# Kernel tuning notes

Measured on AMD Instinct MI355X. Metric: run time of the kernel, lower is better.

## Reference

```python
import jax, jax.numpy as jnp
import numpy as np

N = 50000      # nodes
E = 800000     # edges
NIN = 512      # input features
NHID = 128     # hidden
NCLS = 64      # classes


def setup_inputs() -> dict:
    key = jax.random.key(0)
    k0, k1, k2, k3 = jax.random.split(key, 4)
    x = jax.random.normal(k0, (N, NIN), dtype=jnp.float32)
    edge_index = jax.random.randint(k1, (2, E), 0, N, dtype=jnp.int64)
    # Glorot-style init for GCNConv linear weights (bias starts at zero in PyG)
    W1 = jax.random.normal(k2, (NIN, NHID), dtype=jnp.float32) * (1.0 / np.sqrt(NIN))
    W2 = jax.random.normal(k3, (NHID, NCLS), dtype=jnp.float32) * (1.0 / np.sqrt(NHID))
    b1 = jnp.zeros((NHID,), dtype=jnp.float32)
    b2 = jnp.zeros((NCLS,), dtype=jnp.float32)
    return {"x": x, "edge_index": edge_index, "W1": W1, "b1": b1, "W2": W2, "b2": b2}


def gcn_conv(x, W, b, src, dst, n):
    """PyG GCNConv: linear transform, then sym-normalized aggregation with self-loops."""
    xw = x @ W                                                  # [n, out]
    ones = jnp.ones(src.shape[0], dtype=xw.dtype)
    deg = jax.ops.segment_sum(ones, dst, num_segments=n) + 1.0  # +1 for self-loop
    dinv = jax.lax.rsqrt(deg)                                   # deg >= 1
    norm = dinv[src] * dinv[dst]                                # [E]
    agg = jax.ops.segment_sum(xw[src] * norm[:, None], dst, num_segments=n)
    agg = agg + (dinv * dinv)[:, None] * xw                     # self-loop messages
    return agg + b


def reference(x, edge_index, W1, b1, W2, b2):
    src, dst = edge_index[0], edge_index[1]
    n = x.shape[0]
    # eval mode: dropout is a no-op; bn is defined but unused in forward
    h = gcn_conv(x, W1, b1, src, dst, n)
    h = jax.nn.relu(h)
    o = gcn_conv(h, W2, b2, src, dst, n)
    return jax.nn.log_softmax(o, axis=1)
```

## Files before the change

### kernel.cpp

```cpp
#include <hip/hip_runtime.h>
#include <hip/hip_bf16.h>
#include <cstdint>
#include <cstddef>

#define NNODES 50000
#define NEDGES 800000
#define NIN    512
#define NHID   128
#define NCLS   64

#define SCAN_BLK 512
#define SCAN_NB ((NNODES + SCAN_BLK - 1) / SCAN_BLK)

typedef __attribute__((ext_vector_type(8))) short bf16x8;
typedef __attribute__((ext_vector_type(4))) float f32x4;

static __device__ __forceinline__ ushort f2bf(float f) {
    uint32_t u = __float_as_uint(f);
    uint32_t r = (u + 0x7fffu + ((u >> 16) & 1u)) >> 16;
    return (ushort)r;
}
static __device__ __forceinline__ float bf2f(ushort b) {
    return __uint_as_float(((uint32_t)b) << 16);
}

__global__ void clear_kernel(int4* __restrict__ p, int n4) {
    int i = blockIdx.x * blockDim.x + threadIdx.x;
    if (i < n4) p[i] = make_int4(0, 0, 0, 0);
}


__global__ void deg_kernel(const int* __restrict__ dst, int* __restrict__ deg) {
    int e = blockIdx.x * blockDim.x + threadIdx.x;
    if (e < NEDGES) atomicAdd(&deg[dst[e]], 1);
}

__global__ __launch_bounds__(SCAN_BLK) void scan1_kernel(const int* __restrict__ deg,
                                                         int* __restrict__ blkSum,
                                                         float* __restrict__ dinv) {
    int i = blockIdx.x * SCAN_BLK + threadIdx.x;
    int d = (i < NNODES) ? deg[i] : 0;
    if (i < NNODES) dinv[i] = rsqrtf((float)d + 1.0f);
    int v = d;
#pragma unroll
    for (int off = 32; off; off >>= 1) v += __shfl_xor(v, off, 64);
    __shared__ int ws[SCAN_BLK / 64];
    int w = threadIdx.x >> 6;
    if ((threadIdx.x & 63) == 0) ws[w] = v;
    __syncthreads();
    if (threadIdx.x == 0) {
        int s = 0;
#pragma unroll
        for (int k = 0; k < SCAN_BLK / 64; ++k) s += ws[k];
        blkSum[blockIdx.x] = s;
    }
}

__global__ void scan2_kernel(int* __restrict__ blkSum, int* __restrict__ rowptr) {
    __shared__ int sh[128];
    int t = threadIdx.x;
    int v = (t < SCAN_NB) ? blkSum[t] : 0;
    sh[t] = v;
    __syncthreads();
    for (int off = 1; off < 128; off <<= 1) {
        int o = (t >= off) ? sh[t - off] : 0;
        __syncthreads();
        sh[t] += o;
        __syncthreads();
    }
    if (t < SCAN_NB) blkSum[t] = sh[t] - v;
    if (t == 0) rowptr[NNODES] = NEDGES;
}

__global__ __launch_bounds__(SCAN_BLK) void scan3_kernel(const int* __restrict__ deg,
                                                         const int* __restrict__ blkOff,
                                                         int* __restrict__ rowptr) {
    int i = blockIdx.x * SCAN_BLK + threadIdx.x;
    int v = (i < NNODES) ? deg[i] : 0;
    int lane = threadIdx.x & 63;
    int w = threadIdx.x >> 6;
    int inc = v;
#pragma unroll
    for (int off = 1; off < 64; off <<= 1) {
        int o = __shfl_up(inc, off, 64);
        if (lane >= off) inc += o;
    }
    __shared__ int ws[SCAN_BLK / 64];
    if (lane == 63) ws[w] = inc;
    __syncthreads();
    int wpre = 0;
    for (int k = 0; k < w; ++k) wpre += ws[k];
    if (i < NNODES) rowptr[i] = inc - v + wpre + blkOff[blockIdx.x];
}

__global__ void scatter_kernel(const int* __restrict__ src, const int* __restrict__ dst,
                               const int* __restrict__ rowptr, int* __restrict__ cursor,
                               const float* __restrict__ dinv, int2* __restrict__ csr) {
    int e = blockIdx.x * blockDim.x + threadIdx.x;
    if (e >= NEDGES) return;
    int d = dst[e];
    int s = src[e];
    int pos = rowptr[d] + atomicAdd(&cursor[d], 1);
    csr[pos] = make_int2(s, __float_as_int(dinv[s]));
}

template <int NOUT, int KS, int CF>
__global__ void pack_kernel(const float* __restrict__ W, ushort* __restrict__ pack) {
    int t = blockIdx.x * blockDim.x + threadIdx.x;
    if (t >= KS * CF * 64 * 8) return;
    int j = t & 7;
    int lane = (t >> 3) & 63;
    int cf = (t >> 9) % CF;
    int ks = t / (CF * 512);
    int k = ks * 32 + (lane >> 4) * 8 + j;
    int c = cf * 16 + (lane & 15);
    pack[t] = f2bf(W[(size_t)k * NOUT + c]);
}

__global__ __launch_bounds__(256) void gemm1_kernel(const float* __restrict__ A,
                                                    const ushort* __restrict__ packB,
                                                    ushort* __restrict__ C) {
    __shared__ f32x4 red[3][8][64];
    const int t = threadIdx.x;
    const int lane = t & 63;
    const int w = t >> 6;
    const int rowBase = blockIdx.x * 16;
    const int rl = lane & 15;
    const int kg = lane >> 4;
    const float* ap = A + (size_t)(rowBase + rl) * NIN + w * 128 + kg * 8;

    float4 xv[8];
#pragma unroll
    for (int ks = 0; ks < 4; ++ks) {
        xv[2 * ks]     = *(const float4*)(ap + ks * 32);
        xv[2 * ks + 1] = *(const float4*)(ap + ks * 32 + 4);
    }

    f32x4 acc[8];
#pragma unroll
    for (int cf = 0; cf < 8; ++cf) acc[cf] = (f32x4)(0.f);

#pragma unroll
    for (int ks = 0; ks < 4; ++ks) {
        float4 x0 = xv[2 * ks], x1 = xv[2 * ks + 1];
        bf16x8 af;
        af[0] = (short)f2bf(x0.x); af[1] = (short)f2bf(x0.y);
        af[2] = (short)f2bf(x0.z); af[3] = (short)f2bf(x0.w);
        af[4] = (short)f2bf(x1.x); af[5] = (short)f2bf(x1.y);
        af[6] = (short)f2bf(x1.z); af[7] = (short)f2bf(x1.w);
        const ushort* bp = packB + ((size_t)((w * 4 + ks) * 8) * 64 + lane) * 8;
#pragma unroll
        for (int cf = 0; cf < 8; ++cf) {
            bf16x8 bfv = *(const bf16x8*)(bp + cf * 512);
            acc[cf] = __builtin_amdgcn_mfma_f32_16x16x32_bf16(af, bfv, acc[cf], 0, 0, 0);
        }
    }

    if (w) {
#pragma unroll
        for (int cf = 0; cf < 8; ++cf) red[w - 1][cf][lane] = acc[cf];
    }
    __syncthreads();
    if (w == 0) {
#pragma unroll
        for (int cf = 0; cf < 8; ++cf)
#pragma unroll
            for (int q = 0; q < 3; ++q) {
                f32x4 v = red[q][cf][lane];
                acc[cf][0] += v[0]; acc[cf][1] += v[1];
                acc[cf][2] += v[2]; acc[cf][3] += v[3];
            }
#pragma unroll
        for (int cf = 0; cf < 8; ++cf)
#pragma unroll
            for (int j = 0; j < 4; ++j)
                C[(size_t)(rowBase + kg * 4 + j) * NHID + cf * 16 + rl] = f2bf(acc[cf][j]);
    }
}

__global__ __launch_bounds__(256) void gemm2_kernel(const ushort* __restrict__ A,
                                                    const ushort* __restrict__ packB,
                                                    ushort* __restrict__ C) {
    int wid = (blockIdx.x * blockDim.x + threadIdx.x) >> 6;
    int lane = threadIdx.x & 63;
    int rowBase = wid * 16;
    if (rowBase >= NNODES) return;
    int rl = lane & 15;
    int kg = lane >> 4;
    const ushort* ap = A + (size_t)(rowBase + rl) * NHID + kg * 8;

    f32x4 acc[4];
#pragma unroll
    for (int cf = 0; cf < 4; ++cf) acc[cf] = (f32x4)(0.f);

#pragma unroll
    for (int ks = 0; ks < 4; ++ks) {
        bf16x8 af = *(const bf16x8*)(ap + ks * 32);
        const ushort* bp = packB + ((size_t)(ks * 4) * 64 + lane) * 8;
#pragma unroll
        for (int cf = 0; cf < 4; ++cf) {
            bf16x8 bf = *(const bf16x8*)(bp + (size_t)cf * 512);
            acc[cf] = __builtin_amdgcn_mfma_f32_16x16x32_bf16(af, bf, acc[cf], 0, 0, 0);
        }
    }
#pragma unroll
    for (int cf = 0; cf < 4; ++cf)
#pragma unroll
        for (int j = 0; j < 4; ++j)
            C[(size_t)(rowBase + kg * 4 + j) * NCLS + cf * 16 + rl] = f2bf(acc[cf][j]);
}

__global__ __launch_bounds__(256) void agg1_kernel(const ushort* __restrict__ xw,
                                                   const int* __restrict__ rowptr,
                                                   const int2* __restrict__ csr,
                                                   const float* __restrict__ dinv,
                                                   const float* __restrict__ b1,
                                                   ushort* __restrict__ h) {
    int wid = (blockIdx.x * blockDim.x + threadIdx.x) >> 6;
    int lane = threadIdx.x & 63;
    if (wid >= NNODES) return;
    int beg = rowptr[wid], end = rowptr[wid + 1];
    float a0 = 0.f, a1 = 0.f;
    int j = beg;
    for (; j + 8 <= end; j += 8) {
        int2 e[8];
#pragma unroll
        for (int q = 0; q < 8; ++q) e[q] = csr[j + q];
        uint v[8];
#pragma unroll
        for (int q = 0; q < 8; ++q) v[q] = *(const uint*)&xw[(size_t)e[q].x * NHID + lane * 2];
#pragma unroll
        for (int q = 0; q < 8; ++q) {
            float wq = __int_as_float(e[q].y);
            a0 += wq * __uint_as_float(v[q] << 16);
            a1 += wq * __uint_as_float(v[q] & 0xffff0000u);
        }
    }
    for (; j < end; ++j) {
        int2 e = csr[j];
        float w = __int_as_float(e.y);
        uint v = *(const uint*)&xw[(size_t)e.x * NHID + lane * 2];
        a0 += w * __uint_as_float(v << 16);
        a1 += w * __uint_as_float(v & 0xffff0000u);
    }
    float di = dinv[wid];
    float sl = di * di;
    uint xv = *(const uint*)&xw[(size_t)wid * NHID + lane * 2];
    float2 bv = *(const float2*)&b1[lane * 2];
    float r0 = di * a0 + sl * __uint_as_float(xv << 16) + bv.x;
    float r1 = di * a1 + sl * __uint_as_float(xv & 0xffff0000u) + bv.y;
    uint o = (uint)f2bf(fmaxf(r0, 0.f)) | ((uint)f2bf(fmaxf(r1, 0.f)) << 16);
    *(uint*)&h[(size_t)wid * NHID + lane * 2] = o;
}

__global__ __launch_bounds__(256) void agg2_kernel(const ushort* __restrict__ xw,
                                                   const int* __restrict__ rowptr,
                                                   const int2* __restrict__ csr,
                                                   const float* __restrict__ dinv,
                                                   const float* __restrict__ b2,
                                                   float* __restrict__ out) {
    int wid = (blockIdx.x * blockDim.x + threadIdx.x) >> 6;
    int lane = threadIdx.x & 63;
    if (wid >= NNODES) return;
    int beg = rowptr[wid], end = rowptr[wid + 1];
    float a = 0.f;
    int j = beg;
    for (; j + 8 <= end; j += 8) {
        int2 e[8];
#pragma unroll
        for (int q = 0; q < 8; ++q) e[q] = csr[j + q];
        float v[8];
#pragma unroll
        for (int q = 0; q < 8; ++q) v[q] = bf2f(xw[(size_t)e[q].x * NCLS + lane]);
#pragma unroll
        for (int q = 0; q < 8; ++q) a += __int_as_float(e[q].y) * v[q];
    }
    for (; j < end; ++j) {
        int2 e = csr[j];
        a += __int_as_float(e.y) * bf2f(xw[(size_t)e.x * NCLS + lane]);
    }
    float di = dinv[wid];
    float o = di * a + di * di * bf2f(xw[(size_t)wid * NCLS + lane]) + b2[lane];
    float m = o;
#pragma unroll
    for (int off = 32; off; off >>= 1) m = fmaxf(m, __shfl_xor(m, off, 64));
    float ex = __expf(o - m);
    float ssum = ex;
#pragma unroll
    for (int off = 32; off; off >>= 1) ssum += __shfl_xor(ssum, off, 64);
    out[(size_t)wid * NCLS + lane] = (o - m) - __logf(ssum);
}


extern "C" void kernel_launch(void* const* d_in, const int* in_sizes, int n_in,
                              void* d_out, int out_size, void* d_ws, size_t ws_size,
                              hipStream_t stream) {
    const float* x  = (const float*)d_in[0];
    const int*   ei = (const int*)d_in[1];
    const int*   src = ei;
    const int*   dst = ei + NEDGES;
    const float* W1 = (const float*)d_in[2];
    const float* b1 = (const float*)d_in[3];
    const float* W2 = (const float*)d_in[4];
    const float* b2 = (const float*)d_in[5];
    float* out = (float*)d_out;

    char* w = (char*)d_ws;
    auto alloc = [&](size_t bytes) {
        char* p = w;
        w += (bytes + 255) & ~(size_t)255;
        return p;
    };
    int*    deg    = (int*)alloc((size_t)2 * NNODES * 4);
    int*    cursor = deg + NNODES;
    int*    rowptr = (int*)alloc((NNODES + 1) * 4);
    int*    blkSum = (int*)alloc(SCAN_NB * 4);
    int2*   csr    = (int2*)alloc((size_t)NEDGES * 8);
    float*  dinv   = (float*)alloc(NNODES * 4);
    ushort* pack1  = (ushort*)alloc((size_t)16 * 8 * 64 * 8 * 2);
    ushort* pack2  = (ushort*)alloc((size_t)4 * 4 * 64 * 8 * 2);
    ushort* xw1    = (ushort*)alloc((size_t)NNODES * NHID * 2);
    ushort* h      = (ushort*)alloc((size_t)NNODES * NHID * 2);
    ushort* xw2    = (ushort*)alloc((size_t)NNODES * NCLS * 2);

    const int n4 = (2 * NNODES + 3) / 4;
    clear_kernel<<<(n4 + 255) / 256, 256, 0, stream>>>((int4*)deg, n4);

    deg_kernel<<<(NEDGES + 255) / 256, 256, 0, stream>>>(dst, deg);
    scan1_kernel<<<SCAN_NB, SCAN_BLK, 0, stream>>>(deg, blkSum, dinv);
    scan2_kernel<<<1, 128, 0, stream>>>(blkSum, rowptr);
    scan3_kernel<<<SCAN_NB, SCAN_BLK, 0, stream>>>(deg, blkSum, rowptr);
    scatter_kernel<<<(NEDGES + 255) / 256, 256, 0, stream>>>(src, dst, rowptr, cursor, dinv, csr);

    pack_kernel<NHID, 16, 8><<<(16 * 8 * 64 * 8 + 255) / 256, 256, 0, stream>>>(W1, pack1);
    pack_kernel<NCLS, 4, 4><<<(4 * 4 * 64 * 8 + 255) / 256, 256, 0, stream>>>(W2, pack2);

    gemm1_kernel<<<NNODES / 16, 256, 0, stream>>>(x, pack1, xw1);
    agg1_kernel<<<(NNODES * 64 + 255) / 256, 256, 0, stream>>>(xw1, rowptr, csr, dinv, b1, h);

    gemm2_kernel<<<(NNODES / 16 + 3) / 4, 256, 0, stream>>>(h, pack2, xw2);
    agg2_kernel<<<(NNODES * 64 + 255) / 256, 256, 0, stream>>>(xw2, rowptr, csr, dinv, b2, out);
}
```

Before: 215.7 us.

## Restructure gemm1 into single-wave triple-buffered global-to-LDS pipeline

Measured after the change: 213.0 us. Within noise of the previous version (-1.3%).

```diff
diff --git a/kernel.cpp b/kernel.cpp
--- a/kernel.cpp
+++ b/kernel.cpp
@@ -117,65 +117,79 @@
     pack[t] = f2bf(W[(size_t)k * NOUT + c]);
 }
 
-__global__ __launch_bounds__(256) void gemm1_kernel(const float* __restrict__ A,
-                                                    const ushort* __restrict__ packB,
-                                                    ushort* __restrict__ C) {
-    __shared__ f32x4 red[3][8][64];
-    const int t = threadIdx.x;
-    const int lane = t & 63;
-    const int w = t >> 6;
+__global__ __launch_bounds__(64) void gemm1_kernel(const float* __restrict__ A,
+                                                   const ushort* __restrict__ packB,
+                                                   ushort* __restrict__ C) {
+    __shared__ float lds[3][16 * 64];
+    const int lane = threadIdx.x;
     const int rowBase = blockIdx.x * 16;
     const int rl = lane & 15;
     const int kg = lane >> 4;
-    const float* ap = A + (size_t)(rowBase + rl) * NIN + w * 128 + kg * 8;
-
-    float4 xv[8];
-#pragma unroll
-    for (int ks = 0; ks < 4; ++ks) {
-        xv[2 * ks]     = *(const float4*)(ap + ks * 32);
-        xv[2 * ks + 1] = *(const float4*)(ap + ks * 32 + 4);
-    }
+    const int srow = lane >> 4;
+    const int scol = lane & 15;
+    const char* Abase = (const char*)A + (size_t)rowBase * (NIN * 4);
 
     f32x4 acc[8];
 #pragma unroll
     for (int cf = 0; cf < 8; ++cf) acc[cf] = (f32x4)(0.f);
 
-#pragma unroll
-    for (int ks = 0; ks < 4; ++ks) {
-        float4 x0 = xv[2 * ks], x1 = xv[2 * ks + 1];
-        bf16x8 af;
-        af[0] = (short)f2bf(x0.x); af[1] = (short)f2bf(x0.y);
-        af[2] = (short)f2bf(x0.z); af[3] = (short)f2bf(x0.w);
-        af[4] = (short)f2bf(x1.x); af[5] = (short)f2bf(x1.y);
-        af[6] = (short)f2bf(x1.z); af[7] = (short)f2bf(x1.w);
-        const ushort* bp = packB + ((size_t)((w * 4 + ks) * 8) * 64 + lane) * 8;
-#pragma unroll
-        for (int cf = 0; cf < 8; ++cf) {
-            bf16x8 bfv = *(const bf16x8*)(bp + cf * 512);
-            acc[cf] = __builtin_amdgcn_mfma_f32_16x16x32_bf16(af, bfv, acc[cf], 0, 0, 0);
+    auto stage = [&](int buf, int chunk) {
+#pragma unroll
+        for (int r = 0; r < 4; ++r) {
+            const int row = r * 4 + srow;
+            const char* src = Abase + (size_t)row * (NIN * 4) + chunk * 256
+                              + ((scol ^ (row & 7)) << 4);
+            char* dst = (char*)&lds[buf][0] + r * 1024 + lane * 16;
+            __builtin_amdgcn_global_load_lds((const uint32_t*)src, (uint32_t*)dst, 16, 0, 0);
         }
-    }
-
-    if (w) {
-#pragma unroll
-        for (int cf = 0; cf < 8; ++cf) red[w - 1][cf][lane] = acc[cf];
-    }
-    __syncthreads();
-    if (w == 0) {
-#pragma unroll
-        for (int cf = 0; cf < 8; ++cf)
-#pragma unroll
-            for (int q = 0; q < 3; ++q) {
-                f32x4 v = red[q][cf][lane];
-                acc[cf][0] += v[0]; acc[cf][1] += v[1];
-                acc[cf][2] += v[2]; acc[cf][3] += v[3];
-            }
-#pragma unroll
-        for (int cf = 0; cf < 8; ++cf)
-#pragma unroll
-            for (int j = 0; j < 4; ++j)
-                C[(size_t)(rowBase + kg * 4 + j) * NHID + cf * 16 + rl] = f2bf(acc[cf][j]);
-    }
+    };
+
+    stage(0, 0);
+    stage(1, 1);
+
+#define G1_CHUNK(c, VMSTR)                                                              \
+    {                                                                                   \
+        if ((c) + 2 < 8) {                                                              \
+            asm volatile("s_waitcnt lgkmcnt(0)" ::: "memory");     \
+            stage(((c) + 2) % 3, (c) + 2);                                              \
+        }                                                                               \
+        asm volatile("s_waitcnt " VMSTR ::: "memory");                                  \
+        __builtin_amdgcn_sched_barrier(0);                                              \
+        const char* lrow = (const char*)&lds[(c) % 3][0] + rl * 256;                    \
+        _Pragma("unroll")                                                               \
+        for (int ks = 0; ks < 2; ++ks) {                                                \
+            const int blk = kg * 2 + ks * 8;                                            \
+            float4 x0 = *(const float4*)(lrow + (((blk) ^ (rl & 7)) << 4));             \
+            float4 x1 = *(const float4*)(lrow + (((blk + 1) ^ (rl & 7)) << 4));         \
+            bf16x8 af;                                                                  \
+            af[0] = (short)f2bf(x0.x); af[1] = (short)f2bf(x0.y);                       \
+            af[2] = (short)f2bf(x0.z); af[3] = (short)f2bf(x0.w);                       \
+            af[4] = (short)f2bf(x1.x); af[5] = (short)f2bf(x1.y);                       \
+            af[6] = (short)f2bf(x1.z); af[7] = (short)f2bf(x1.w);                       \
+            const ushort* bpp = packB + ((size_t)(((c) * 2 + ks) * 8) * 64 + lane) * 8; \
+            _Pragma("unroll")                                                           \
+            for (int cf = 0; cf < 8; ++cf) {                                            \
+                bf16x8 bfv = *(const bf16x8*)(bpp + cf * 512);                          \
+                acc[cf] = __builtin_amdgcn_mfma_f32_16x16x32_bf16(af, bfv, acc[cf], 0, 0, 0); \
+            }                                                                           \
+        }                                                                               \
+    }
+
+    G1_CHUNK(0, "vmcnt(8)")
+    G1_CHUNK(1, "vmcnt(8)")
+    G1_CHUNK(2, "vmcnt(8)")
+    G1_CHUNK(3, "vmcnt(8)")
+    G1_CHUNK(4, "vmcnt(8)")
+    G1_CHUNK(5, "vmcnt(8)")
+    G1_CHUNK(6, "vmcnt(4)")
+    G1_CHUNK(7, "vmcnt(0)")
+#undef G1_CHUNK
+
+#pragma unroll
+    for (int cf = 0; cf < 8; ++cf)
+#pragma unroll
+        for (int j = 0; j < 4; ++j)
+            C[(size_t)(rowBase + kg * 4 + j) * NHID + cf * 16 + rl] = f2bf(acc[cf][j]);
 }
 
 __global__ __launch_bounds__(256) void gemm2_kernel(const ushort* __restrict__ A,
@@ -335,7 +349,7 @@
     pack_kernel<NHID, 16, 8><<<(16 * 8 * 64 * 8 + 255) / 256, 256, 0, stream>>>(W1, pack1);
     pack_kernel<NCLS, 4, 4><<<(4 * 4 * 64 * 8 + 255) / 256, 256, 0, stream>>>(W2, pack2);
 
-    gemm1_kernel<<<NNODES / 16, 256, 0, stream>>>(x, pack1, xw1);
+    gemm1_kernel<<<NNODES / 16, 64, 0, stream>>>(x, pack1, xw1);
     agg1_kernel<<<(NNODES * 64 + 255) / 256, 256, 0, stream>>>(xw1, rowptr, csr, dinv, b1, h);
 
     gemm2_kernel<<<(NNODES / 16 + 3) / 4, 256, 0, stream>>>(h, pack2, xw2);
```
